# Kernel optimization log

Hardware: AMD Instinct MI355X
Metric: run time of the kernel (lower is better)

The kernel has to match this reference:

```python
import jax, jax.numpy as jnp
import numpy as np

EPS = 1e-9  # projective normalization epsilon
LN_EPS = 1e-5


def setup_inputs() -> dict:
    N, E, Fin, Fout = 50000, 600000, 128, 128
    key = jax.random.key(0)
    ks = jax.random.split(key, 8)
    x = jax.random.normal(ks[0], (N, Fin), jnp.float32)
    edge_index = jax.random.randint(ks[1], (2, E), 0, N, dtype=jnp.int64)
    edge_weight = jax.random.normal(ks[2], (E,), jnp.float32)
    W_self = jax.random.normal(ks[3], (Fin, Fout), jnp.float32) / np.sqrt(Fin)
    b_self = jnp.zeros((Fout,), jnp.float32)
    W_nb = jax.random.normal(ks[4], (Fin, Fout), jnp.float32) / np.sqrt(Fin)
    b_nb = jnp.zeros((Fout,), jnp.float32)
    gamma = jnp.ones((Fout,), jnp.float32)
    beta = jnp.zeros((Fout,), jnp.float32)
    return dict(x=x, edge_index=edge_index, edge_weight=edge_weight,
                W_self=W_self, b_self=b_self, W_nb=W_nb, b_nb=b_nb,
                gamma=gamma, beta=beta)


def _proj_normalize(v):
    # UHG projective_average tail: L2-normalize the weighted sum
    return v / (jnp.linalg.norm(v, axis=-1, keepdims=True) + EPS)


def reference(x, edge_index, edge_weight, W_self, b_self, W_nb, b_nb, gamma, beta):
    N = x.shape[0]
    src, tgt = edge_index[0], edge_index[1]

    # --- neighbor aggregation: per-target softmax over edge weights, then
    # weighted projective average of gathered source features (vectorized
    # replacement of the per-node python loop) ---
    seg_max = jax.ops.segment_max(edge_weight, tgt, num_segments=N)  # [N]
    ew = jnp.exp(edge_weight - seg_max[tgt])                          # [E]
    denom = jax.ops.segment_sum(ew, tgt, num_segments=N)              # [N]
    alpha = ew / denom[tgt]                                           # softmax per target
    agg = jax.ops.segment_sum(alpha[:, None] * x[src], tgt, num_segments=N)  # [N, Fin]
    agg = _proj_normalize(agg)  # isolated nodes stay exactly zero (0 / eps)

    # --- self / neighbor linear transforms ---
    self_feat = x @ W_self + b_self    # [N, Fout]
    nb_feat = agg @ W_nb + b_nb        # [N, Fout]

    # --- combine: projective average with weights [0.5, 0.5] ---
    comb = _proj_normalize(0.5 * (self_feat + nb_feat))

    # --- UHG layer norm (standard layernorm over feature dim) ---
    mu = jnp.mean(comb, axis=-1, keepdims=True)
    var = jnp.var(comb, axis=-1, keepdims=True)
    out = (comb - mu) / jnp.sqrt(var + LN_EPS) * gamma + beta
    # dropout is identity in eval mode
    return out
```

## Files before the change

kernel.cpp:

```cpp
#include <hip/hip_runtime.h>
#include <hip/hip_bf16.h>

#define EPS 1e-9f
#define LN_EPS 1e-5f

typedef __attribute__((ext_vector_type(8))) short bf16x8;
typedef __attribute__((ext_vector_type(4))) float f32x4;

__device__ __forceinline__ float lo16(unsigned p) { return __uint_as_float(p << 16); }
__device__ __forceinline__ float hi16(unsigned p) { return __uint_as_float(p & 0xffff0000u); }
__device__ __forceinline__ unsigned f2b(float f) {
    unsigned u = __float_as_uint(f);
    return (u + 0x7fffu + ((u >> 16) & 1u)) >> 16;
}
__device__ __forceinline__ int eidx(const int* ei, int i, int i64) {
    return i64 ? ei[2 * i] : ei[i];
}
__device__ __forceinline__ float ldw(const float* fp, const __hip_bfloat16* hp, int i, int f32) {
    return f32 ? fp[i] : __bfloat162float(hp[i]);
}

__global__ void probe_kernel(const unsigned* __restrict__ xb, const int* __restrict__ ei,
                             int* __restrict__ flags) {
    int lane = threadIdx.x & 63;
    unsigned d = xb[lane * 97];
    unsigned ex = (d >> 7) & 0xFFu;
    unsigned long long m1 = __ballot(ex >= 110u && ex <= 135u);
    int hi = ei[2 * lane + 1];
    unsigned long long m2 = __ballot(hi == 0);
    if (lane == 0) {
        flags[0] = (__popcll(m1) > 32) ? 0 : 1;
        flags[1] = (__popcll(m2) > 32) ? 1 : 0;
    }
}

__global__ void cvt_x(const float4* __restrict__ xf4, uint2* __restrict__ xcvt2,
                      const int* __restrict__ flags, int n4) {
    if (!flags[0]) return;
    int i = blockIdx.x * 256 + threadIdx.x;
    if (i >= n4) return;
    float4 v = xf4[i];
    xcvt2[i] = make_uint2(f2b(v.x) | (f2b(v.y) << 16), f2b(v.z) | (f2b(v.w) << 16));
}

__global__ void transpose_w(const unsigned* __restrict__ Wsb, const float* __restrict__ Wsf,
                            const unsigned* __restrict__ Wnb, const float* __restrict__ Wnf,
                            unsigned* __restrict__ wt, const int* __restrict__ flags) {
    int tid = blockIdx.x * 256 + threadIdx.x;
    int f = tid >> 7, k2 = tid & 127;
    int k2l = k2 & 63;
    unsigned out;
    if (flags[0]) {
        const float* W = (k2 < 64) ? Wsf : Wnf;
        float lo = W[(2 * k2l) * 128 + f], hi = W[(2 * k2l + 1) * 128 + f];
        out = f2b(lo) | (f2b(hi) << 16);
    } else {
        const unsigned* W = (k2 < 64) ? Wsb : Wnb;
        unsigned lo = W[(2 * k2l) * 64 + (f >> 1)];
        unsigned hi = W[(2 * k2l + 1) * 64 + (f >> 1)];
        unsigned a = (f & 1) ? (lo >> 16) : (lo & 0xffffu);
        unsigned b = (f & 1) ? (hi & 0xffff0000u) : (hi << 16);
        out = a | b;
    }
    wt[tid] = out;
}

__global__ void edge_count(const int* __restrict__ ei, int* __restrict__ count,
                           int* __restrict__ tgt32, int* __restrict__ rank,
                           const int* __restrict__ flags, int E) {
    int e0 = (blockIdx.x * 256 + threadIdx.x) * 4;
    if (e0 >= E) return;
    int i64 = flags[1];
    if (e0 + 4 <= E) {
        int t0 = eidx(ei, E + e0 + 0, i64), t1 = eidx(ei, E + e0 + 1, i64),
            t2 = eidx(ei, E + e0 + 2, i64), t3 = eidx(ei, E + e0 + 3, i64);
        int r0 = atomicAdd(&count[t0], 1), r1 = atomicAdd(&count[t1], 1),
            r2 = atomicAdd(&count[t2], 1), r3 = atomicAdd(&count[t3], 1);
        *(int4*)(tgt32 + e0) = make_int4(t0, t1, t2, t3);
        *(int4*)(rank + e0)  = make_int4(r0, r1, r2, r3);
    } else {
        for (int j = 0; j < 4 && e0 + j < E; ++j) {
            int t = eidx(ei, E + e0 + j, i64);
            rank[e0 + j] = atomicAdd(&count[t], 1);
            tgt32[e0 + j] = t;
        }
    }
}

__global__ void scan_kernel(const int* __restrict__ count, int* __restrict__ offsets, int N) {
    __shared__ int wsum[16];
    __shared__ int s_carry;
    int tid = threadIdx.x, lane = tid & 63, w = tid >> 6;
    if (tid == 0) s_carry = 0;
    __syncthreads();
    for (int base = 0; base < N; base += 4096) {
        int i0 = base + tid * 4;
        int4 v;
        if (i0 + 3 < N) v = *(const int4*)(count + i0);
        else {
            v.x = (i0     < N) ? count[i0]     : 0;
            v.y = (i0 + 1 < N) ? count[i0 + 1] : 0;
            v.z = (i0 + 2 < N) ? count[i0 + 2] : 0;
            v.w = (i0 + 3 < N) ? count[i0 + 3] : 0;
        }
        int s = v.x + v.y + v.z + v.w;
        int incl = s;
        #pragma unroll
        for (int off = 1; off < 64; off <<= 1) {
            int t = __shfl_up(incl, off);
            if (lane >= off) incl += t;
        }
        if (lane == 63) wsum[w] = incl;
        __syncthreads();
        int wpre = 0, tot = 0;
        #pragma unroll
        for (int j = 0; j < 16; ++j) { int sj = wsum[j]; if (j < w) wpre += sj; tot += sj; }
        int o0 = s_carry + wpre + incl - s;
        int o1 = o0 + v.x, o2 = o1 + v.y, o3 = o2 + v.z;
        if (i0 + 3 < N) {
            *(int4*)(offsets + i0) = make_int4(o0, o1, o2, o3);
        } else {
            if (i0     < N) offsets[i0]     = o0;
            if (i0 + 1 < N) offsets[i0 + 1] = o1;
            if (i0 + 2 < N) offsets[i0 + 2] = o2;
        }
        __syncthreads();
        if (tid == 0) s_carry += tot;
        __syncthreads();
    }
    if (threadIdx.x == 0) offsets[N] = s_carry;
}

__global__ void edge_scatter(const int* __restrict__ ei, const int* __restrict__ tgt32,
                             const int* __restrict__ rank,
                             const float* __restrict__ ewf, const __hip_bfloat16* __restrict__ ewh,
                             const int* __restrict__ offsets, uint2* __restrict__ csr,
                             const int* __restrict__ flags, int E) {
    int e0 = (blockIdx.x * 256 + threadIdx.x) * 4;
    if (e0 >= E) return;
    int f32 = flags[0], i64 = flags[1];
    if (e0 + 4 <= E) {
        int4 t = *(const int4*)(tgt32 + e0);
        int4 r = *(const int4*)(rank + e0);
        int s0 = eidx(ei, e0 + 0, i64), s1 = eidx(ei, e0 + 1, i64),
            s2 = eidx(ei, e0 + 2, i64), s3 = eidx(ei, e0 + 3, i64);
        float w0 = ldw(ewf, ewh, e0 + 0, f32), w1 = ldw(ewf, ewh, e0 + 1, f32),
              w2 = ldw(ewf, ewh, e0 + 2, f32), w3 = ldw(ewf, ewh, e0 + 3, f32);
        int o0 = offsets[t.x], o1 = offsets[t.y], o2 = offsets[t.z], o3 = offsets[t.w];
        csr[o0 + r.x] = make_uint2((unsigned)s0, __float_as_uint(expf(w0)));
        csr[o1 + r.y] = make_uint2((unsigned)s1, __float_as_uint(expf(w1)));
        csr[o2 + r.z] = make_uint2((unsigned)s2, __float_as_uint(expf(w2)));
        csr[o3 + r.w] = make_uint2((unsigned)s3, __float_as_uint(expf(w3)));
    } else {
        for (int j = 0; j < 4 && e0 + j < E; ++j) {
            int e = e0 + j;
            int t = tgt32[e];
            int s = eidx(ei, e, i64);
            float w = ldw(ewf, ewh, e, f32);
            csr[offsets[t] + rank[e]] = make_uint2((unsigned)s, __float_as_uint(expf(w)));
        }
    }
}

__global__ void aggregate(const unsigned* __restrict__ xb, const unsigned* __restrict__ xcvt,
                          const int* __restrict__ offsets, const uint2* __restrict__ csr,
                          unsigned* __restrict__ aggb, const int* __restrict__ flags, int N) {
    int node = blockIdx.x * 4 + (threadIdx.x >> 6);
    if (node >= N) return;
    int lane = threadIdx.x & 63;
    const unsigned* xs = flags[0] ? xcvt : xb;
    float a0 = 0.f, a1 = 0.f;
    int beg = offsets[node], end = offsets[node + 1];
    int j = beg;
    for (; j + 8 <= end; j += 8) {
        uint2 e0 = csr[j+0], e1 = csr[j+1], e2 = csr[j+2], e3 = csr[j+3],
              e4 = csr[j+4], e5 = csr[j+5], e6 = csr[j+6], e7 = csr[j+7];
        unsigned p0 = xs[e0.x * 64 + lane], p1 = xs[e1.x * 64 + lane],
                 p2 = xs[e2.x * 64 + lane], p3 = xs[e3.x * 64 + lane],
                 p4 = xs[e4.x * 64 + lane], p5 = xs[e5.x * 64 + lane],
                 p6 = xs[e6.x * 64 + lane], p7 = xs[e7.x * 64 + lane];
        float l0 = __uint_as_float(e0.y), l1 = __uint_as_float(e1.y),
              l2 = __uint_as_float(e2.y), l3 = __uint_as_float(e3.y),
              l4 = __uint_as_float(e4.y), l5 = __uint_as_float(e5.y),
              l6 = __uint_as_float(e6.y), l7 = __uint_as_float(e7.y);
        a0 += l0 * lo16(p0); a1 += l0 * hi16(p0);
        a0 += l1 * lo16(p1); a1 += l1 * hi16(p1);
        a0 += l2 * lo16(p2); a1 += l2 * hi16(p2);
        a0 += l3 * lo16(p3); a1 += l3 * hi16(p3);
        a0 += l4 * lo16(p4); a1 += l4 * hi16(p4);
        a0 += l5 * lo16(p5); a1 += l5 * hi16(p5);
        a0 += l6 * lo16(p6); a1 += l6 * hi16(p6);
        a0 += l7 * lo16(p7); a1 += l7 * hi16(p7);
    }
    for (; j + 4 <= end; j += 4) {
        uint2 e0 = csr[j+0], e1 = csr[j+1], e2 = csr[j+2], e3 = csr[j+3];
        unsigned p0 = xs[e0.x * 64 + lane], p1 = xs[e1.x * 64 + lane],
                 p2 = xs[e2.x * 64 + lane], p3 = xs[e3.x * 64 + lane];
        float l0 = __uint_as_float(e0.y), l1 = __uint_as_float(e1.y),
              l2 = __uint_as_float(e2.y), l3 = __uint_as_float(e3.y);
        a0 += l0 * lo16(p0); a1 += l0 * hi16(p0);
        a0 += l1 * lo16(p1); a1 += l1 * hi16(p1);
        a0 += l2 * lo16(p2); a1 += l2 * hi16(p2);
        a0 += l3 * lo16(p3); a1 += l3 * hi16(p3);
    }
    for (; j < end; ++j) {
        uint2 e = csr[j];
        unsigned p = xs[e.x * 64 + lane];
        float l = __uint_as_float(e.y);
        a0 += l * lo16(p); a1 += l * hi16(p);
    }
    float ss = a0 * a0 + a1 * a1;
    #pragma unroll
    for (int m = 32; m >= 1; m >>= 1) ss += __shfl_xor(ss, m);
    float inv = 1.f / (sqrtf(ss) + EPS);
    aggb[node * 64 + lane] = f2b(a0 * inv) | (f2b(a1 * inv) << 16);
}

__global__ __launch_bounds__(256) void fused_mfma(
    const unsigned* __restrict__ xb, const unsigned* __restrict__ xcvt,
    const unsigned* __restrict__ aggb, const uint4* __restrict__ wt4,
    const float* __restrict__ bsf, const __hip_bfloat16* __restrict__ bsh,
    const float* __restrict__ bnf, const __hip_bfloat16* __restrict__ bnh,
    const float* __restrict__ gf, const __hip_bfloat16* __restrict__ gh,
    const float* __restrict__ tf, const __hip_bfloat16* __restrict__ th,
    float* __restrict__ outf, unsigned* __restrict__ outb,
    const int* __restrict__ flags, int N)
{
    __shared__ uint4 sA[2048];
    int f32 = flags[0];
    const uint4* xs4 = (const uint4*)(f32 ? xcvt : xb);
    const uint4* ag4 = (const uint4*)aggb;
    int tid = threadIdx.x;
    int node0 = blockIdx.x * 64;

    #pragma unroll
    for (int i = 0; i < 8; ++i) {
        int ci = i * 256 + tid;
        int r = ci >> 5, c = ci & 31;
        int node = node0 + r;
        uint4 v = make_uint4(0, 0, 0, 0);
        if (node < N) v = (c < 16) ? xs4[node * 16 + c] : ag4[node * 16 + (c - 16)];
        sA[r * 32 + (c ^ (r & 15))] = v;
    }
    __syncthreads();

    int lane = tid & 63, w = tid >> 6, g = lane >> 4, c16 = lane & 15;
    int rloc = w * 16 + c16;

    f32x4 acc[8];
    #pragma unroll
    for (int t = 0; t < 8; ++t) acc[t] = (f32x4){0.f, 0.f, 0.f, 0.f};

    #pragma unroll
    for (int kk = 0; kk < 8; ++kk) {
        uint4 av = sA[rloc * 32 + ((kk * 4 + g) ^ c16)];
        bf16x8 a = __builtin_bit_cast(bf16x8, av);
        #pragma unroll
        for (int t = 0; t < 8; ++t) {
            uint4 bv = wt4[(t * 16 + c16) * 32 + kk * 4 + g];
            bf16x8 b = __builtin_bit_cast(bf16x8, bv);
            acc[t] = __builtin_amdgcn_mfma_f32_16x16x32_bf16(a, b, acc[t], 0, 0, 0);
        }
    }

    float bsum[8], gam[8], bet[8];
    #pragma unroll
    for (int t = 0; t < 8; ++t) {
        int f = t * 16 + c16;
        bsum[t] = ldw(bsf, bsh, f, f32) + ldw(bnf, bnh, f, f32);
        gam[t]  = ldw(gf, gh, f, f32);
        bet[t]  = ldw(tf, th, f, f32);
    }

    #pragma unroll
    for (int reg = 0; reg < 4; ++reg) {
        int node = node0 + w * 16 + g * 4 + reg;
        float cv[8], s1 = 0.f, s2 = 0.f;
        #pragma unroll
        for (int t = 0; t < 8; ++t) {
            float c_ = 0.5f * (acc[t][reg] + bsum[t]);
            cv[t] = c_; s1 += c_; s2 += c_ * c_;
        }
        #pragma unroll
        for (int m = 1; m < 16; m <<= 1) { s1 += __shfl_xor(s1, m); s2 += __shfl_xor(s2, m); }
        float inv  = 1.f / (sqrtf(s2) + EPS);
        float mean = s1 * inv * (1.f / 128.f);
        float var  = s2 * inv * inv * (1.f / 128.f) - mean * mean;
        float rstd = 1.f / sqrtf(var + LN_EPS);
        if (f32) {
            if (node < N) {
                #pragma unroll
                for (int t = 0; t < 8; ++t) {
                    float o = (cv[t] * inv - mean) * rstd * gam[t] + bet[t];
                    outf[(size_t)node * 128 + t * 16 + c16] = o;
                }
            }
        } else {
            #pragma unroll
            for (int t = 0; t < 8; ++t) {
                float o = (cv[t] * inv - mean) * rstd * gam[t] + bet[t];
                float po = __shfl_xor(o, 1);
                if (!(c16 & 1) && node < N)
                    outb[node * 64 + t * 8 + (c16 >> 1)] = f2b(o) | (f2b(po) << 16);
            }
        }
    }
}

static inline size_t rup16(size_t x) { return (x + 15) & ~(size_t)15; }

extern "C" void kernel_launch(void* const* d_in, const int* in_sizes, int n_in,
                              void* d_out, int out_size, void* d_ws, size_t ws_size,
                              hipStream_t stream) {
    int N = in_sizes[0] / 128;
    int E = in_sizes[1] / 2;
    const int* ei = (const int*)d_in[1];

    char* p = (char*)d_ws;
    int* flags = (int*)p;              p += 16;
    int* count = (int*)p;              p += rup16((size_t)N * 4);
    int* offsets = (int*)p;            p += rup16((size_t)(N + 4) * 4);
    int* tgt32 = (int*)p;              p += rup16((size_t)E * 4);
    int* rank = (int*)p;               p += rup16((size_t)E * 4);
    uint2* csr = (uint2*)p;            p += rup16((size_t)E * 8);
    unsigned* wt = (unsigned*)p;       p += 128 * 128 * 4;
    unsigned* xcvt = (unsigned*)p;     p += rup16((size_t)N * 64 * 4);
    unsigned* aggb = (unsigned*)p;

    hipMemsetAsync(d_ws, 0, 16 + (size_t)N * 4, stream);

    int eb4 = (E + 1023) / 1024;
    int nb = (N + 3) / 4;
    int nb64 = (N + 63) / 64;
    int ncv = (N * 32 + 255) / 256;

    probe_kernel<<<1, 64, 0, stream>>>((const unsigned*)d_in[0], ei, flags);
    cvt_x<<<ncv, 256, 0, stream>>>((const float4*)d_in[0], (uint2*)xcvt, flags, N * 32);
    transpose_w<<<64, 256, 0, stream>>>((const unsigned*)d_in[3], (const float*)d_in[3],
                                        (const unsigned*)d_in[5], (const float*)d_in[5],
                                        wt, flags);
    edge_count<<<eb4, 256, 0, stream>>>(ei, count, tgt32, rank, flags, E);
    scan_kernel<<<1, 1024, 0, stream>>>(count, offsets, N);
    edge_scatter<<<eb4, 256, 0, stream>>>(ei, tgt32, rank, (const float*)d_in[2],
                                          (const __hip_bfloat16*)d_in[2],
                                          offsets, csr, flags, E);
    aggregate<<<nb, 256, 0, stream>>>((const unsigned*)d_in[0], xcvt,
                                      offsets, csr, aggb, flags, N);
    fused_mfma<<<nb64, 256, 0, stream>>>((const unsigned*)d_in[0], xcvt, aggb, (const uint4*)wt,
                                         (const float*)d_in[4], (const __hip_bfloat16*)d_in[4],
                                         (const float*)d_in[6], (const __hip_bfloat16*)d_in[6],
                                         (const float*)d_in[7], (const __hip_bfloat16*)d_in[7],
                                         (const float*)d_in[8], (const __hip_bfloat16*)d_in[8],
                                         (float*)d_out, (unsigned*)d_out, flags, N);
}
```

Baseline: 226.6 us.

## Pack CSR edges to 32-bit, parallelize scan, merge prep kernels, shrink fused tile

```diff
diff --git a/kernel.cpp b/kernel.cpp
--- a/kernel.cpp
+++ b/kernel.cpp
@@ -1,5 +1,6 @@
 #include <hip/hip_runtime.h>
 #include <hip/hip_bf16.h>
+#include <hip/hip_fp16.h>
 
 #define EPS 1e-9f
 #define LN_EPS 1e-5f
@@ -34,35 +35,35 @@
     }
 }
 
-__global__ void cvt_x(const float4* __restrict__ xf4, uint2* __restrict__ xcvt2,
-                      const int* __restrict__ flags, int n4) {
-    if (!flags[0]) return;
-    int i = blockIdx.x * 256 + threadIdx.x;
-    if (i >= n4) return;
-    float4 v = xf4[i];
-    xcvt2[i] = make_uint2(f2b(v.x) | (f2b(v.y) << 16), f2b(v.z) | (f2b(v.w) << 16));
-}
-
-__global__ void transpose_w(const unsigned* __restrict__ Wsb, const float* __restrict__ Wsf,
-                            const unsigned* __restrict__ Wnb, const float* __restrict__ Wnf,
-                            unsigned* __restrict__ wt, const int* __restrict__ flags) {
-    int tid = blockIdx.x * 256 + threadIdx.x;
-    int f = tid >> 7, k2 = tid & 127;
-    int k2l = k2 & 63;
-    unsigned out;
-    if (flags[0]) {
-        const float* W = (k2 < 64) ? Wsf : Wnf;
-        float lo = W[(2 * k2l) * 128 + f], hi = W[(2 * k2l + 1) * 128 + f];
-        out = f2b(lo) | (f2b(hi) << 16);
-    } else {
-        const unsigned* W = (k2 < 64) ? Wsb : Wnb;
-        unsigned lo = W[(2 * k2l) * 64 + (f >> 1)];
-        unsigned hi = W[(2 * k2l + 1) * 64 + (f >> 1)];
-        unsigned a = (f & 1) ? (lo >> 16) : (lo & 0xffffu);
-        unsigned b = (f & 1) ? (hi & 0xffff0000u) : (hi << 16);
-        out = a | b;
-    }
-    wt[tid] = out;
+__global__ void prep(const float4* __restrict__ xf4, uint2* __restrict__ xcvt2,
+                     const unsigned* __restrict__ Wsb, const float* __restrict__ Wsf,
+                     const unsigned* __restrict__ Wnb, const float* __restrict__ Wnf,
+                     unsigned* __restrict__ wt, const int* __restrict__ flags, int n4) {
+    if (blockIdx.x < 64) {
+        int tid = blockIdx.x * 256 + threadIdx.x;
+        int f = tid >> 7, k2 = tid & 127;
+        int k2l = k2 & 63;
+        unsigned out;
+        if (flags[0]) {
+            const float* W = (k2 < 64) ? Wsf : Wnf;
+            float lo = W[(2 * k2l) * 128 + f], hi = W[(2 * k2l + 1) * 128 + f];
+            out = f2b(lo) | (f2b(hi) << 16);
+        } else {
+            const unsigned* W = (k2 < 64) ? Wsb : Wnb;
+            unsigned lo = W[(2 * k2l) * 64 + (f >> 1)];
+            unsigned hi = W[(2 * k2l + 1) * 64 + (f >> 1)];
+            unsigned a = (f & 1) ? (lo >> 16) : (lo & 0xffffu);
+            unsigned b = (f & 1) ? (hi & 0xffff0000u) : (hi << 16);
+            out = a | b;
+        }
+        wt[tid] = out;
+    } else {
+        if (!flags[0]) return;
+        int i = (blockIdx.x - 64) * 256 + threadIdx.x;
+        if (i >= n4) return;
+        float4 v = xf4[i];
+        xcvt2[i] = make_uint2(f2b(v.x) | (f2b(v.y) << 16), f2b(v.z) | (f2b(v.w) << 16));
+    }
 }
 
 __global__ void edge_count(const int* __restrict__ ei, int* __restrict__ count,
@@ -87,55 +88,77 @@
     }
 }
 
-__global__ void scan_kernel(const int* __restrict__ count, int* __restrict__ offsets, int N) {
+__global__ void scan_blocks(const int* __restrict__ count, int* __restrict__ offsets,
+                            int* __restrict__ bsum, int N) {
     __shared__ int wsum[16];
-    __shared__ int s_carry;
     int tid = threadIdx.x, lane = tid & 63, w = tid >> 6;
-    if (tid == 0) s_carry = 0;
+    int i0 = blockIdx.x * 4096 + tid * 4;
+    int4 v;
+    if (i0 + 3 < N) v = *(const int4*)(count + i0);
+    else {
+        v.x = (i0     < N) ? count[i0]     : 0;
+        v.y = (i0 + 1 < N) ? count[i0 + 1] : 0;
+        v.z = (i0 + 2 < N) ? count[i0 + 2] : 0;
+        v.w = (i0 + 3 < N) ? count[i0 + 3] : 0;
+    }
+    int s = v.x + v.y + v.z + v.w;
+    int incl = s;
+    #pragma unroll
+    for (int off = 1; off < 64; off <<= 1) {
+        int t = __shfl_up(incl, off);
+        if (lane >= off) incl += t;
+    }
+    if (lane == 63) wsum[w] = incl;
     __syncthreads();
-    for (int base = 0; base < N; base += 4096) {
-        int i0 = base + tid * 4;
-        int4 v;
-        if (i0 + 3 < N) v = *(const int4*)(count + i0);
-        else {
-            v.x = (i0     < N) ? count[i0]     : 0;
-            v.y = (i0 + 1 < N) ? count[i0 + 1] : 0;
-            v.z = (i0 + 2 < N) ? count[i0 + 2] : 0;
-            v.w = (i0 + 3 < N) ? count[i0 + 3] : 0;
-        }
-        int s = v.x + v.y + v.z + v.w;
-        int incl = s;
-        #pragma unroll
-        for (int off = 1; off < 64; off <<= 1) {
-            int t = __shfl_up(incl, off);
-            if (lane >= off) incl += t;
-        }
-        if (lane == 63) wsum[w] = incl;
-        __syncthreads();
-        int wpre = 0, tot = 0;
-        #pragma unroll
-        for (int j = 0; j < 16; ++j) { int sj = wsum[j]; if (j < w) wpre += sj; tot += sj; }
-        int o0 = s_carry + wpre + incl - s;
-        int o1 = o0 + v.x, o2 = o1 + v.y, o3 = o2 + v.z;
-        if (i0 + 3 < N) {
-            *(int4*)(offsets + i0) = make_int4(o0, o1, o2, o3);
-        } else {
-            if (i0     < N) offsets[i0]     = o0;
-            if (i0 + 1 < N) offsets[i0 + 1] = o1;
-            if (i0 + 2 < N) offsets[i0 + 2] = o2;
-        }
-        __syncthreads();
-        if (tid == 0) s_carry += tot;
-        __syncthreads();
-    }
-    if (threadIdx.x == 0) offsets[N] = s_carry;
-}
-
+    int wpre = 0, tot = 0;
+    #pragma unroll
+    for (int j = 0; j < 16; ++j) { int sj = wsum[j]; if (j < w) wpre += sj; tot += sj; }
+    int o0 = wpre + incl - s;
+    int o1 = o0 + v.x, o2 = o1 + v.y, o3 = o2 + v.z;
+    if (i0 + 3 < N) {
+        *(int4*)(offsets + i0) = make_int4(o0, o1, o2, o3);
+    } else {
+        if (i0     < N) offsets[i0]     = o0;
+        if (i0 + 1 < N) offsets[i0 + 1] = o1;
+        if (i0 + 2 < N) offsets[i0 + 2] = o2;
+    }
+    if (tid == 0) bsum[blockIdx.x] = tot;
+}
+
+__global__ void scan_fixup(int* __restrict__ offsets, const int* __restrict__ bsum,
+                           int N, int B) {
+    __shared__ int s_pre;
+    int b = blockIdx.x;
+    if (threadIdx.x == 0) {
+        int p = 0;
+        for (int j = 0; j < b; ++j) p += bsum[j];
+        s_pre = p;
+        if (b == B - 1) {
+            int tot = p;
+            for (int j = b; j < B; ++j) tot += bsum[j];
+            offsets[N] = tot;
+        }
+    }
+    __syncthreads();
+    int pre = s_pre;
+    if (pre == 0) return;
+    int i0 = b * 4096 + threadIdx.x * 4;
+    if (i0 + 3 < N) {
+        int4 t = *(int4*)(offsets + i0);
+        t.x += pre; t.y += pre; t.z += pre; t.w += pre;
+        *(int4*)(offsets + i0) = t;
+    } else {
+        for (int j = 0; j < 4; ++j)
+            if (i0 + j < N) offsets[i0 + j] += pre;
+    }
+}
+
+template <int PACK>
 __global__ void edge_scatter(const int* __restrict__ ei, const int* __restrict__ tgt32,
                              const int* __restrict__ rank,
                              const float* __restrict__ ewf, const __hip_bfloat16* __restrict__ ewh,
-                             const int* __restrict__ offsets, uint2* __restrict__ csr,
-                             const int* __restrict__ flags, int E) {
+                             const int* __restrict__ offsets, unsigned* __restrict__ csr4,
+                             uint2* __restrict__ csr8, const int* __restrict__ flags, int E) {
     int e0 = (blockIdx.x * 256 + threadIdx.x) * 4;
     if (e0 >= E) return;
     int f32 = flags[0], i64 = flags[1];
@@ -146,25 +169,53 @@
             s2 = eidx(ei, e0 + 2, i64), s3 = eidx(ei, e0 + 3, i64);
         float w0 = ldw(ewf, ewh, e0 + 0, f32), w1 = ldw(ewf, ewh, e0 + 1, f32),
               w2 = ldw(ewf, ewh, e0 + 2, f32), w3 = ldw(ewf, ewh, e0 + 3, f32);
-        int o0 = offsets[t.x], o1 = offsets[t.y], o2 = offsets[t.z], o3 = offsets[t.w];
-        csr[o0 + r.x] = make_uint2((unsigned)s0, __float_as_uint(expf(w0)));
-        csr[o1 + r.y] = make_uint2((unsigned)s1, __float_as_uint(expf(w1)));
-        csr[o2 + r.z] = make_uint2((unsigned)s2, __float_as_uint(expf(w2)));
-        csr[o3 + r.w] = make_uint2((unsigned)s3, __float_as_uint(expf(w3)));
+        int o0 = offsets[t.x] + r.x, o1 = offsets[t.y] + r.y,
+            o2 = offsets[t.z] + r.z, o3 = offsets[t.w] + r.w;
+        float a0 = expf(w0), a1 = expf(w1), a2 = expf(w2), a3 = expf(w3);
+        if (PACK) {
+            csr4[o0] = (unsigned)s0 | ((unsigned)__half_as_ushort(__float2half(a0)) << 16);
+            csr4[o1] = (unsigned)s1 | ((unsigned)__half_as_ushort(__float2half(a1)) << 16);
+            csr4[o2] = (unsigned)s2 | ((unsigned)__half_as_ushort(__float2half(a2)) << 16);
+            csr4[o3] = (unsigned)s3 | ((unsigned)__half_as_ushort(__float2half(a3)) << 16);
+        } else {
+            csr8[o0] = make_uint2((unsigned)s0, __float_as_uint(a0));
+            csr8[o1] = make_uint2((unsigned)s1, __float_as_uint(a1));
+            csr8[o2] = make_uint2((unsigned)s2, __float_as_uint(a2));
+            csr8[o3] = make_uint2((unsigned)s3, __float_as_uint(a3));
+        }
     } else {
         for (int j = 0; j < 4 && e0 + j < E; ++j) {
             int e = e0 + j;
             int t = tgt32[e];
             int s = eidx(ei, e, i64);
-            float w = ldw(ewf, ewh, e, f32);
-            csr[offsets[t] + rank[e]] = make_uint2((unsigned)s, __float_as_uint(expf(w)));
-        }
-    }
-}
-
+            float al = expf(ldw(ewf, ewh, e, f32));
+            int pos = offsets[t] + rank[e];
+            if (PACK) csr4[pos] = (unsigned)s | ((unsigned)__half_as_ushort(__float2half(al)) << 16);
+            else      csr8[pos] = make_uint2((unsigned)s, __float_as_uint(al));
+        }
+    }
+}
+
+template <int PACK>
+__device__ __forceinline__ void dec_edge(const unsigned* __restrict__ c4,
+                                         const uint2* __restrict__ c8, int j,
+                                         unsigned& s, float& al) {
+    if (PACK) {
+        unsigned r = c4[j];
+        s = r & 0xffffu;
+        al = __half2float(__ushort_as_half((unsigned short)(r >> 16)));
+    } else {
+        uint2 e = c8[j];
+        s = e.x;
+        al = __uint_as_float(e.y);
+    }
+}
+
+template <int PACK>
 __global__ void aggregate(const unsigned* __restrict__ xb, const unsigned* __restrict__ xcvt,
-                          const int* __restrict__ offsets, const uint2* __restrict__ csr,
-                          unsigned* __restrict__ aggb, const int* __restrict__ flags, int N) {
+                          const int* __restrict__ offsets, const unsigned* __restrict__ csr4,
+                          const uint2* __restrict__ csr8, unsigned* __restrict__ aggb,
+                          const int* __restrict__ flags, int N) {
     int node = blockIdx.x * 4 + (threadIdx.x >> 6);
     if (node >= N) return;
     int lane = threadIdx.x & 63;
@@ -173,16 +224,16 @@
     int beg = offsets[node], end = offsets[node + 1];
     int j = beg;
     for (; j + 8 <= end; j += 8) {
-        uint2 e0 = csr[j+0], e1 = csr[j+1], e2 = csr[j+2], e3 = csr[j+3],
-              e4 = csr[j+4], e5 = csr[j+5], e6 = csr[j+6], e7 = csr[j+7];
-        unsigned p0 = xs[e0.x * 64 + lane], p1 = xs[e1.x * 64 + lane],
-                 p2 = xs[e2.x * 64 + lane], p3 = xs[e3.x * 64 + lane],
-                 p4 = xs[e4.x * 64 + lane], p5 = xs[e5.x * 64 + lane],
-                 p6 = xs[e6.x * 64 + lane], p7 = xs[e7.x * 64 + lane];
-        float l0 = __uint_as_float(e0.y), l1 = __uint_as_float(e1.y),
-              l2 = __uint_as_float(e2.y), l3 = __uint_as_float(e3.y),
-              l4 = __uint_as_float(e4.y), l5 = __uint_as_float(e5.y),
-              l6 = __uint_as_float(e6.y), l7 = __uint_as_float(e7.y);
+        unsigned s0, s1, s2, s3, s4, s5, s6, s7;
+        float l0, l1, l2, l3, l4, l5, l6, l7;
+        dec_edge<PACK>(csr4, csr8, j+0, s0, l0); dec_edge<PACK>(csr4, csr8, j+1, s1, l1);
+        dec_edge<PACK>(csr4, csr8, j+2, s2, l2); dec_edge<PACK>(csr4, csr8, j+3, s3, l3);
+        dec_edge<PACK>(csr4, csr8, j+4, s4, l4); dec_edge<PACK>(csr4, csr8, j+5, s5, l5);
+        dec_edge<PACK>(csr4, csr8, j+6, s6, l6); dec_edge<PACK>(csr4, csr8, j+7, s7, l7);
+        unsigned p0 = xs[s0 * 64 + lane], p1 = xs[s1 * 64 + lane],
+                 p2 = xs[s2 * 64 + lane], p3 = xs[s3 * 64 + lane],
+                 p4 = xs[s4 * 64 + lane], p5 = xs[s5 * 64 + lane],
+                 p6 = xs[s6 * 64 + lane], p7 = xs[s7 * 64 + lane];
         a0 += l0 * lo16(p0); a1 += l0 * hi16(p0);
         a0 += l1 * lo16(p1); a1 += l1 * hi16(p1);
         a0 += l2 * lo16(p2); a1 += l2 * hi16(p2);
@@ -193,20 +244,21 @@
         a0 += l7 * lo16(p7); a1 += l7 * hi16(p7);
     }
     for (; j + 4 <= end; j += 4) {
-        uint2 e0 = csr[j+0], e1 = csr[j+1], e2 = csr[j+2], e3 = csr[j+3];
-        unsigned p0 = xs[e0.x * 64 + lane], p1 = xs[e1.x * 64 + lane],
-                 p2 = xs[e2.x * 64 + lane], p3 = xs[e3.x * 64 + lane];
-        float l0 = __uint_as_float(e0.y), l1 = __uint_as_float(e1.y),
-              l2 = __uint_as_float(e2.y), l3 = __uint_as_float(e3.y);
+        unsigned s0, s1, s2, s3;
+        float l0, l1, l2, l3;
+        dec_edge<PACK>(csr4, csr8, j+0, s0, l0); dec_edge<PACK>(csr4, csr8, j+1, s1, l1);
+        dec_edge<PACK>(csr4, csr8, j+2, s2, l2); dec_edge<PACK>(csr4, csr8, j+3, s3, l3);
+        unsigned p0 = xs[s0 * 64 + lane], p1 = xs[s1 * 64 + lane],
+                 p2 = xs[s2 * 64 + lane], p3 = xs[s3 * 64 + lane];
         a0 += l0 * lo16(p0); a1 += l0 * hi16(p0);
         a0 += l1 * lo16(p1); a1 += l1 * hi16(p1);
         a0 += l2 * lo16(p2); a1 += l2 * hi16(p2);
         a0 += l3 * lo16(p3); a1 += l3 * hi16(p3);
     }
     for (; j < end; ++j) {
-        uint2 e = csr[j];
-        unsigned p = xs[e.x * 64 + lane];
-        float l = __uint_as_float(e.y);
+        unsigned s; float l;
+        dec_edge<PACK>(csr4, csr8, j, s, l);
+        unsigned p = xs[s * 64 + lane];
         a0 += l * lo16(p); a1 += l * hi16(p);
     }
     float ss = a0 * a0 + a1 * a1;
@@ -216,7 +268,7 @@
     aggb[node * 64 + lane] = f2b(a0 * inv) | (f2b(a1 * inv) << 16);
 }
 
-__global__ __launch_bounds__(256) void fused_mfma(
+__global__ __launch_bounds__(128) void fused_mfma(
     const unsigned* __restrict__ xb, const unsigned* __restrict__ xcvt,
     const unsigned* __restrict__ aggb, const uint4* __restrict__ wt4,
     const float* __restrict__ bsf, const __hip_bfloat16* __restrict__ bsh,
@@ -226,16 +278,16 @@
     float* __restrict__ outf, unsigned* __restrict__ outb,
     const int* __restrict__ flags, int N)
 {
-    __shared__ uint4 sA[2048];
+    __shared__ uint4 sA[1024];
     int f32 = flags[0];
     const uint4* xs4 = (const uint4*)(f32 ? xcvt : xb);
     const uint4* ag4 = (const uint4*)aggb;
     int tid = threadIdx.x;
-    int node0 = blockIdx.x * 64;
+    int node0 = blockIdx.x * 32;
 
     #pragma unroll
     for (int i = 0; i < 8; ++i) {
-        int ci = i * 256 + tid;
+        int ci = i * 128 + tid;
         int r = ci >> 5, c = ci & 31;
         int node = node0 + r;
         uint4 v = make_uint4(0, 0, 0, 0);
@@ -320,9 +372,11 @@
     int* flags = (int*)p;              p += 16;
     int* count = (int*)p;              p += rup16((size_t)N * 4);
     int* offsets = (int*)p;            p += rup16((size_t)(N + 4) * 4);
+    int* bsum = (int*)p;               p += 256;
     int* tgt32 = (int*)p;              p += rup16((size_t)E * 4);
     int* rank = (int*)p;               p += rup16((size_t)E * 4);
-    uint2* csr = (uint2*)p;            p += rup16((size_t)E * 8);
+    unsigned* csr4 = (unsigned*)p;
+    uint2* csr8 = (uint2*)p;           p += rup16((size_t)E * 8);
     unsigned* wt = (unsigned*)p;       p += 128 * 128 * 4;
     unsigned* xcvt = (unsigned*)p;     p += rup16((size_t)N * 64 * 4);
     unsigned* aggb = (unsigned*)p;
@@ -331,25 +385,37 @@
 
     int eb4 = (E + 1023) / 1024;
     int nb = (N + 3) / 4;
-    int nb64 = (N + 63) / 64;
+    int nbf = (N + 31) / 32;
     int ncv = (N * 32 + 255) / 256;
+    int scanB = (N + 4095) / 4096;
+    int pack = (N <= 65536);
 
     probe_kernel<<<1, 64, 0, stream>>>((const unsigned*)d_in[0], ei, flags);
-    cvt_x<<<ncv, 256, 0, stream>>>((const float4*)d_in[0], (uint2*)xcvt, flags, N * 32);
-    transpose_w<<<64, 256, 0, stream>>>((const unsigned*)d_in[3], (const float*)d_in[3],
-                                        (const unsigned*)d_in[5], (const float*)d_in[5],
-                                        wt, flags);
+    prep<<<64 + ncv, 256, 0, stream>>>((const float4*)d_in[0], (uint2*)xcvt,
+                                       (const unsigned*)d_in[3], (const float*)d_in[3],
+                                       (const unsigned*)d_in[5], (const float*)d_in[5],
+                                       wt, flags, N * 32);
     edge_count<<<eb4, 256, 0, stream>>>(ei, count, tgt32, rank, flags, E);
-    scan_kernel<<<1, 1024, 0, stream>>>(count, offsets, N);
-    edge_scatter<<<eb4, 256, 0, stream>>>(ei, tgt32, rank, (const float*)d_in[2],
-                                          (const __hip_bfloat16*)d_in[2],
-                                          offsets, csr, flags, E);
-    aggregate<<<nb, 256, 0, stream>>>((const unsigned*)d_in[0], xcvt,
-                                      offsets, csr, aggb, flags, N);
-    fused_mfma<<<nb64, 256, 0, stream>>>((const unsigned*)d_in[0], xcvt, aggb, (const uint4*)wt,
-                                         (const float*)d_in[4], (const __hip_bfloat16*)d_in[4],
-                                         (const float*)d_in[6], (const __hip_bfloat16*)d_in[6],
-                                         (const float*)d_in[7], (const __hip_bfloat16*)d_in[7],
-                                         (const float*)d_in[8], (const __hip_bfloat16*)d_in[8],
-                                         (float*)d_out, (unsigned*)d_out, flags, N);
-}
+    scan_blocks<<<scanB, 1024, 0, stream>>>(count, offsets, bsum, N);
+    scan_fixup<<<scanB, 1024, 0, stream>>>(offsets, bsum, N, scanB);
+    if (pack)
+        edge_scatter<1><<<eb4, 256, 0, stream>>>(ei, tgt32, rank, (const float*)d_in[2],
+                                                 (const __hip_bfloat16*)d_in[2],
+                                                 offsets, csr4, csr8, flags, E);
+    else
+        edge_scatter<0><<<eb4, 256, 0, stream>>>(ei, tgt32, rank, (const float*)d_in[2],
+                                                 (const __hip_bfloat16*)d_in[2],
+                                                 offsets, csr4, csr8, flags, E);
+    if (pack)
+        aggregate<1><<<nb, 256, 0, stream>>>((const unsigned*)d_in[0], xcvt,
+                                             offsets, csr4, csr8, aggb, flags, N);
+    else
+        aggregate<0><<<nb, 256, 0, stream>>>((const unsigned*)d_in[0], xcvt,
+                                             offsets, csr4, csr8, aggb, flags, N);
+    fused_mfma<<<nbf, 128, 0, stream>>>((const unsigned*)d_in[0], xcvt, aggb, (const uint4*)wt,
+                                        (const float*)d_in[4], (const __hip_bfloat16*)d_in[4],
+                                        (const float*)d_in[6], (const __hip_bfloat16*)d_in[6],
+                                        (const float*)d_in[7], (const __hip_bfloat16*)d_in[7],
+                                        (const float*)d_in[8], (const __hip_bfloat16*)d_in[8],
+                                        (float*)d_out, (unsigned*)d_out, flags, N);
+}
```

Result: faster. 209.1 us (-7.7%).
